# Optimization experiments

Hardware: AMD Instinct MI355X
Metric: run time of the kernel (lower is better)

## Reference

```python
import jax, jax.numpy as jnp
import numpy as np
import math


def butterfly_mult_untied(twiddle, x, increasing_stride=True):
    """twiddle: (nstack, m, n//2, 2, 2); x: (batch, nstack, n)."""
    b, nstack, n = x.shape
    m = twiddle.shape[1]
    out = x
    for idx in range(m):  # loop over log2(n) stages (structural, not data dim)
        log_stride = idx if increasing_stride else m - 1 - idx
        stride = 1 << log_stride
        nb = n // (2 * stride)
        # (nstack, nb, stride, 2, 2) -> (nstack, nb, 2, 2, stride)
        t = jnp.transpose(twiddle[:, idx].reshape(nstack, nb, stride, 2, 2), (0, 1, 3, 4, 2))
        o = out.reshape(b, nstack, nb, 1, 2, stride)
        out = (t * o).sum(axis=4).reshape(b, nstack, n)
    return out


def setup_inputs() -> dict:
    key = jax.random.key(0)
    k1, k2, k3 = jax.random.split(key, 3)
    batch, in_size, out_size = 32768, 1024, 1024
    m = int(math.ceil(math.log2(in_size)))  # 10
    nstack = 1
    x = jax.random.normal(k1, (batch, in_size), dtype=jnp.float32)
    # 'regular' non-ortho init: randn / sqrt(2)
    twiddle = jax.random.normal(k2, (nstack, m, in_size // 2, 2, 2), dtype=jnp.float32) / math.sqrt(2)
    bound = 1 / math.sqrt(in_size)
    bias = jax.random.uniform(k3, (out_size,), dtype=jnp.float32, minval=-bound, maxval=bound)
    return {"x": x, "twiddle": twiddle, "bias": bias}


def reference(x, twiddle, bias):
    batch, in_size = x.shape
    nstack = twiddle.shape[0]
    out_size = bias.shape[0]
    # pre_process: in_size is a power of 2 and nstack==1 -> just stack
    out = jnp.broadcast_to(x[:, None, :], (batch, nstack, in_size))
    out = butterfly_mult_untied(twiddle, out, increasing_stride=True)
    # post_process: flatten nstack, slice to out_size, add bias
    out = out.reshape(batch, nstack * in_size)[:, :out_size] + bias
    return out
```

## Files before the change

### kernel.cpp

```cpp
#include <hip/hip_runtime.h>


constexpr int N = 1024;
constexpr int B_ROWS = 4;
constexpr int WAVES = 4;

template<int STAGE>
__device__ __forceinline__ void do_stage(float2 (&v)[2][16],
                                         const float* __restrict__ tw,
                                         const int lane)
{
    constexpr int s = 1 << STAGE;
    const float* tws = tw + (STAGE << 11);

    if constexpr (s >= 4 && s <= 128) {
        constexpr int m = s >> 2;
        #pragma unroll
        for (int p = 0; p < 16; ++p) {
            const int e  = ((p >> 2) << 8) | (lane << 2) | (p & 3);
            const int i  = (e >> STAGE) & 1;
            const int pr = ((e >> (STAGE + 1)) << STAGE) | (e & (s - 1));
            const float2 tt = *(const float2*)(tws + pr * 4 + i * 2);
            const float tA = i ? tt.y : tt.x;
            const float tB = i ? tt.x : tt.y;
            #pragma unroll
            for (int q = 0; q < 2; ++q) {
                const float px = __shfl_xor(v[q][p].x, m, 64);
                const float py = __shfl_xor(v[q][p].y, m, 64);
                v[q][p].x = tA * v[q][p].x + tB * px;
                v[q][p].y = tA * v[q][p].y + tB * py;
            }
        }
    } else {
        constexpr int pm = (s == 1) ? 1 : (s == 2) ? 2 : (s == 256) ? 4 : 8;
        #pragma unroll
        for (int p = 0; p < 16; ++p) {
            if (p & pm) continue;
            const int p2 = p | pm;
            const int e  = ((p >> 2) << 8) | (lane << 2) | (p & 3);
            const int pr = ((e >> (STAGE + 1)) << STAGE) | (e & (s - 1));
            const float4 t4 = *(const float4*)(tws + pr * 4);
            #pragma unroll
            for (int q = 0; q < 2; ++q) {
                const float2 a = v[q][p];
                const float2 b = v[q][p2];
                v[q][p].x  = t4.x * a.x + t4.y * b.x;
                v[q][p].y  = t4.x * a.y + t4.y * b.y;
                v[q][p2].x = t4.z * a.x + t4.w * b.x;
                v[q][p2].y = t4.z * a.y + t4.w * b.y;
            }
        }
    }
}

__global__ __launch_bounds__(256, 2)
void butterfly_kernel(const float* __restrict__ x,
                      const float* __restrict__ tw,
                      const float* __restrict__ bias,
                      float* __restrict__ out)
{
    const int lane  = threadIdx.x & 63;
    const int waveg = blockIdx.x * WAVES + (threadIdx.x >> 6);
    const size_t row0 = (size_t)waveg * B_ROWS;

    float2 v[2][16];

    #pragma unroll
    for (int q = 0; q < 2; ++q) {
        const float* p0 = x + (row0 + 2 * q) * N + lane * 4;
        const float* p1 = p0 + N;
        #pragma unroll
        for (int r = 0; r < 4; ++r) {
            const float4 a = *(const float4*)(p0 + r * 256);
            const float4 b = *(const float4*)(p1 + r * 256);
            v[q][r * 4 + 0] = make_float2(a.x, b.x);
            v[q][r * 4 + 1] = make_float2(a.y, b.y);
            v[q][r * 4 + 2] = make_float2(a.z, b.z);
            v[q][r * 4 + 3] = make_float2(a.w, b.w);
        }
    }

    do_stage<0>(v, tw, lane);
    do_stage<1>(v, tw, lane);
    do_stage<2>(v, tw, lane);
    do_stage<3>(v, tw, lane);
    do_stage<4>(v, tw, lane);
    do_stage<5>(v, tw, lane);
    do_stage<6>(v, tw, lane);
    do_stage<7>(v, tw, lane);
    do_stage<8>(v, tw, lane);
    do_stage<9>(v, tw, lane);

    #pragma unroll
    for (int q = 0; q < 2; ++q) {
        float* o0 = out + (row0 + 2 * q) * N + lane * 4;
        float* o1 = o0 + N;
        #pragma unroll
        for (int r = 0; r < 4; ++r) {
            const float4 bb = *(const float4*)(bias + r * 256 + lane * 4);
            float4 a, b;
            a.x = v[q][r * 4 + 0].x + bb.x;  b.x = v[q][r * 4 + 0].y + bb.x;
            a.y = v[q][r * 4 + 1].x + bb.y;  b.y = v[q][r * 4 + 1].y + bb.y;
            a.z = v[q][r * 4 + 2].x + bb.z;  b.z = v[q][r * 4 + 2].y + bb.z;
            a.w = v[q][r * 4 + 3].x + bb.w;  b.w = v[q][r * 4 + 3].y + bb.w;
            *(float4*)(o0 + r * 256) = a;
            *(float4*)(o1 + r * 256) = b;
        }
    }
}

extern "C" void kernel_launch(void* const* d_in, const int* in_sizes, int n_in,
                              void* d_out, int out_size, void* d_ws, size_t ws_size,
                              hipStream_t stream) {
    const float* x    = (const float*)d_in[0];
    const float* tw   = (const float*)d_in[1];
    const float* bias = (const float*)d_in[2];
    float* out        = (float*)d_out;

    const int batch = in_sizes[0] / N;
    const int blocks = batch / (B_ROWS * WAVES);
    hipLaunchKernelGGL(butterfly_kernel, dim3(blocks), dim3(256), 0, stream,
                       x, tw, bias, out);
}
```

Measured before the change: 282.7 us.

## Stage twiddles in shared memory and double-buffer row chunks per wave

Each block now precomputes the pre-swapped twiddle pairs for stages 2-7 into a 48KB LDS table, so those stages do one contiguous float2 LDS read instead of index arithmetic plus a global load and select. Each wave processes four chunks of four rows with two register buffers, loading the next chunk while computing the current one, and the bias is loaded once per wave. Blocks grow from 16 to 64 rows and launch bounds drop to one block per SIMD. This doubles register pressure and LDS use, which may lower occupancy, and adds the table-building cost to every block.

```diff
diff --git a/kernel.cpp b/kernel.cpp
--- a/kernel.cpp
+++ b/kernel.cpp
@@ -2,37 +2,36 @@
 
 
 constexpr int N = 1024;
-constexpr int B_ROWS = 4;
-constexpr int WAVES = 4;
+constexpr int CHUNKS = 4;
+constexpr int ROWS_PER_CHUNK = 16;
+constexpr int ROWS_PER_BLOCK = CHUNKS * ROWS_PER_CHUNK;
+
 
 template<int STAGE>
 __device__ __forceinline__ void do_stage(float2 (&v)[2][16],
+                                         const float* __restrict__ tl,
                                          const float* __restrict__ tw,
                                          const int lane)
 {
     constexpr int s = 1 << STAGE;
-    const float* tws = tw + (STAGE << 11);
 
     if constexpr (s >= 4 && s <= 128) {
         constexpr int m = s >> 2;
+        const float* base = tl + (STAGE - 2) * 2048;
         #pragma unroll
         for (int p = 0; p < 16; ++p) {
-            const int e  = ((p >> 2) << 8) | (lane << 2) | (p & 3);
-            const int i  = (e >> STAGE) & 1;
-            const int pr = ((e >> (STAGE + 1)) << STAGE) | (e & (s - 1));
-            const float2 tt = *(const float2*)(tws + pr * 4 + i * 2);
-            const float tA = i ? tt.y : tt.x;
-            const float tB = i ? tt.x : tt.y;
+            const float2 tt = *(const float2*)(base + (((p << 6) | lane) << 1));
             #pragma unroll
             for (int q = 0; q < 2; ++q) {
                 const float px = __shfl_xor(v[q][p].x, m, 64);
                 const float py = __shfl_xor(v[q][p].y, m, 64);
-                v[q][p].x = tA * v[q][p].x + tB * px;
-                v[q][p].y = tA * v[q][p].y + tB * py;
+                v[q][p].x = tt.x * v[q][p].x + tt.y * px;
+                v[q][p].y = tt.x * v[q][p].y + tt.y * py;
             }
         }
     } else {
         constexpr int pm = (s == 1) ? 1 : (s == 2) ? 2 : (s == 256) ? 4 : 8;
+        const float* tws = tw + (STAGE << 11);
         #pragma unroll
         for (int p = 0; p < 16; ++p) {
             if (p & pm) continue;
@@ -53,18 +52,10 @@
     }
 }
 
-__global__ __launch_bounds__(256, 2)
-void butterfly_kernel(const float* __restrict__ x,
-                      const float* __restrict__ tw,
-                      const float* __restrict__ bias,
-                      float* __restrict__ out)
+__device__ __forceinline__ void load_rows(float2 (&v)[2][16],
+                                          const float* __restrict__ x,
+                                          const size_t row0, const int lane)
 {
-    const int lane  = threadIdx.x & 63;
-    const int waveg = blockIdx.x * WAVES + (threadIdx.x >> 6);
-    const size_t row0 = (size_t)waveg * B_ROWS;
-
-    float2 v[2][16];
-
     #pragma unroll
     for (int q = 0; q < 2; ++q) {
         const float* p0 = x + (row0 + 2 * q) * N + lane * 4;
@@ -79,17 +70,25 @@
             v[q][r * 4 + 3] = make_float2(a.w, b.w);
         }
     }
+}
 
-    do_stage<0>(v, tw, lane);
-    do_stage<1>(v, tw, lane);
-    do_stage<2>(v, tw, lane);
-    do_stage<3>(v, tw, lane);
-    do_stage<4>(v, tw, lane);
-    do_stage<5>(v, tw, lane);
-    do_stage<6>(v, tw, lane);
-    do_stage<7>(v, tw, lane);
-    do_stage<8>(v, tw, lane);
-    do_stage<9>(v, tw, lane);
+__device__ __forceinline__ void compute_store(float2 (&v)[2][16],
+                                              const float* __restrict__ tl,
+                                              const float* __restrict__ tw,
+                                              float* __restrict__ out,
+                                              const size_t row0, const int lane,
+                                              const float4 (&bb)[4])
+{
+    do_stage<0>(v, tl, tw, lane);
+    do_stage<1>(v, tl, tw, lane);
+    do_stage<2>(v, tl, tw, lane);
+    do_stage<3>(v, tl, tw, lane);
+    do_stage<4>(v, tl, tw, lane);
+    do_stage<5>(v, tl, tw, lane);
+    do_stage<6>(v, tl, tw, lane);
+    do_stage<7>(v, tl, tw, lane);
+    do_stage<8>(v, tl, tw, lane);
+    do_stage<9>(v, tl, tw, lane);
 
     #pragma unroll
     for (int q = 0; q < 2; ++q) {
@@ -97,16 +96,62 @@
         float* o1 = o0 + N;
         #pragma unroll
         for (int r = 0; r < 4; ++r) {
-            const float4 bb = *(const float4*)(bias + r * 256 + lane * 4);
             float4 a, b;
-            a.x = v[q][r * 4 + 0].x + bb.x;  b.x = v[q][r * 4 + 0].y + bb.x;
-            a.y = v[q][r * 4 + 1].x + bb.y;  b.y = v[q][r * 4 + 1].y + bb.y;
-            a.z = v[q][r * 4 + 2].x + bb.z;  b.z = v[q][r * 4 + 2].y + bb.z;
-            a.w = v[q][r * 4 + 3].x + bb.w;  b.w = v[q][r * 4 + 3].y + bb.w;
+            a.x = v[q][r * 4 + 0].x + bb[r].x;  b.x = v[q][r * 4 + 0].y + bb[r].x;
+            a.y = v[q][r * 4 + 1].x + bb[r].y;  b.y = v[q][r * 4 + 1].y + bb[r].y;
+            a.z = v[q][r * 4 + 2].x + bb[r].z;  b.z = v[q][r * 4 + 2].y + bb[r].z;
+            a.w = v[q][r * 4 + 3].x + bb[r].w;  b.w = v[q][r * 4 + 3].y + bb[r].w;
             *(float4*)(o0 + r * 256) = a;
             *(float4*)(o1 + r * 256) = b;
         }
     }
+}
+
+__global__ __launch_bounds__(256, 1)
+void butterfly_kernel(const float* __restrict__ x,
+                      const float* __restrict__ tw,
+                      const float* __restrict__ bias,
+                      float* __restrict__ out)
+{
+    __shared__ __align__(16) float tl[6 * 2048];
+
+    const int t    = threadIdx.x;
+    const int lane = t & 63;
+    const int g    = t >> 6;
+
+    #pragma unroll
+    for (int st = 2; st <= 7; ++st) {
+        const int s = 1 << st;
+        #pragma unroll
+        for (int k = 0; k < 4; ++k) {
+            const int p  = (g << 2) | k;
+            const int e  = ((p >> 2) << 8) | (lane << 2) | (p & 3);
+            const int i  = (e >> st) & 1;
+            const int pr = ((e >> (st + 1)) << st) | (e & (s - 1));
+            const float2 tt = *(const float2*)(tw + (st << 11) + pr * 4 + i * 2);
+            const float2 w  = i ? make_float2(tt.y, tt.x) : tt;
+            *(float2*)(tl + (st - 2) * 2048 + (((p << 6) | lane) << 1)) = w;
+        }
+    }
+
+    float4 bb[4];
+    #pragma unroll
+    for (int r = 0; r < 4; ++r)
+        bb[r] = *(const float4*)(bias + r * 256 + lane * 4);
+
+    __syncthreads();
+
+    const size_t base = (size_t)blockIdx.x * ROWS_PER_BLOCK + (size_t)(g * 4);
+
+    float2 vA[2][16], vB[2][16];
+    load_rows(vA, x, base + 0 * ROWS_PER_CHUNK, lane);
+    load_rows(vB, x, base + 1 * ROWS_PER_CHUNK, lane);
+    compute_store(vA, tl, tw, out, base + 0 * ROWS_PER_CHUNK, lane, bb);
+    load_rows(vA, x, base + 2 * ROWS_PER_CHUNK, lane);
+    compute_store(vB, tl, tw, out, base + 1 * ROWS_PER_CHUNK, lane, bb);
+    load_rows(vB, x, base + 3 * ROWS_PER_CHUNK, lane);
+    compute_store(vA, tl, tw, out, base + 2 * ROWS_PER_CHUNK, lane, bb);
+    compute_store(vB, tl, tw, out, base + 3 * ROWS_PER_CHUNK, lane, bb);
 }
 
 extern "C" void kernel_launch(void* const* d_in, const int* in_sizes, int n_in,
@@ -117,8 +162,8 @@
     const float* bias = (const float*)d_in[2];
     float* out        = (float*)d_out;
 
-    const int batch = in_sizes[0] / N;
-    const int blocks = batch / (B_ROWS * WAVES);
+    const int batch  = in_sizes[0] / N;
+    const int blocks = batch / ROWS_PER_BLOCK;
     hipLaunchKernelGGL(butterfly_kernel, dim3(blocks), dim3(256), 0, stream,
                        x, tw, bias, out);
 }
```

Measured after the change: 593.6 us. 110% more time.

## Replace wave shuffles with per-wave LDS transposes between butterfly stage groups

Applied to the files above, without the earlier changes.

Each lane now holds 16 contiguous elements per row, so stages 0-3 run entirely in registers. Two padded LDS transposes inside each wave's private buffer regroup the data so that stages 4-7 and then 8-9 are also register-local. This removes the many cross-lane shuffle instructions and the per-element twiddle selects of the old layout. In exchange it adds LDS traffic and about 21KB of shared memory per block, and it relies on wave-synchronous LDS access with no barrier.

```diff
diff --git a/kernel.cpp b/kernel.cpp
--- a/kernel.cpp
+++ b/kernel.cpp
@@ -4,51 +4,78 @@
 constexpr int N = 1024;
 constexpr int B_ROWS = 4;
 constexpr int WAVES = 4;
+constexpr int WBUF  = 1344;
 
-template<int STAGE>
-__device__ __forceinline__ void do_stage(float2 (&v)[2][16],
-                                         const float* __restrict__ tw,
-                                         const int lane)
+
+template<int ST>
+__device__ __forceinline__ void stageA(float (&v)[4][16],
+                                       const float4* __restrict__ tw4,
+                                       const int lane)
 {
-    constexpr int s = 1 << STAGE;
-    const float* tws = tw + (STAGE << 11);
+    constexpr int s = 1 << ST;
+    #pragma unroll
+    for (int pi = 0; pi < 8; ++pi) {
+        const int jl = ((pi >> ST) << (ST + 1)) | (pi & (s - 1));
+        const int jh = jl + s;
+        const int e  = 16 * lane + jl;
+        const int pr = ((e >> (ST + 1)) << ST) | (e & (s - 1));
+        const float4 t = tw4[ST * 512 + pr];
+        #pragma unroll
+        for (int r = 0; r < 4; ++r) {
+            const float lo = v[r][jl], hi = v[r][jh];
+            v[r][jl] = t.x * lo + t.y * hi;
+            v[r][jh] = t.z * lo + t.w * hi;
+        }
+    }
+}
 
-    if constexpr (s >= 4 && s <= 128) {
-        constexpr int m = s >> 2;
+template<int ST>
+__device__ __forceinline__ void stageE(float (&v)[4][16],
+                                       const float4* __restrict__ tw4,
+                                       const int lane)
+{
+    constexpr int s  = 1 << ST;
+    constexpr int km = 1 << (ST - 4);
+    const int a = lane >> 4, b = lane & 15;
+    #pragma unroll
+    for (int pi = 0; pi < 8; ++pi) {
+        const int kl = ((pi >> (ST - 4)) << (ST - 3)) | (pi & (km - 1));
+        const int kh = kl + km;
+        const int e  = 256 * a + 16 * kl + b;
+        const int pr = ((e >> (ST + 1)) << ST) | (e & (s - 1));
+        const float4 t = tw4[ST * 512 + pr];
         #pragma unroll
-        for (int p = 0; p < 16; ++p) {
-            const int e  = ((p >> 2) << 8) | (lane << 2) | (p & 3);
-            const int i  = (e >> STAGE) & 1;
-            const int pr = ((e >> (STAGE + 1)) << STAGE) | (e & (s - 1));
-            const float2 tt = *(const float2*)(tws + pr * 4 + i * 2);
-            const float tA = i ? tt.y : tt.x;
-            const float tB = i ? tt.x : tt.y;
-            #pragma unroll
-            for (int q = 0; q < 2; ++q) {
-                const float px = __shfl_xor(v[q][p].x, m, 64);
-                const float py = __shfl_xor(v[q][p].y, m, 64);
-                v[q][p].x = tA * v[q][p].x + tB * px;
-                v[q][p].y = tA * v[q][p].y + tB * py;
-            }
+        for (int r = 0; r < 4; ++r) {
+            const float lo = v[r][kl], hi = v[r][kh];
+            v[r][kl] = t.x * lo + t.y * hi;
+            v[r][kh] = t.z * lo + t.w * hi;
         }
-    } else {
-        constexpr int pm = (s == 1) ? 1 : (s == 2) ? 2 : (s == 256) ? 4 : 8;
+    }
+}
+
+template<int ST>
+__device__ __forceinline__ void stageF(float (&v)[4][16],
+                                       const float4* __restrict__ tw4,
+                                       const int lane)
+{
+    constexpr int s  = 1 << ST;
+    constexpr int am = 1 << (ST - 8);
+    #pragma unroll
+    for (int pi = 0; pi < 8; ++pi) {
+        const int ai   = pi >> 2;
+        const int b10  = pi & 3;
+        const int a_lo = ((ai >> (ST - 8)) << (ST - 7)) | (ai & (am - 1));
+        const int a_hi = a_lo + am;
+        const int ml   = a_lo * 4 + b10;
+        const int mh   = a_hi * 4 + b10;
+        const int e    = a_lo * 256 + 4 * lane + b10;
+        const int pr   = ((e >> (ST + 1)) << ST) | (e & (s - 1));
+        const float4 t = tw4[ST * 512 + pr];
         #pragma unroll
-        for (int p = 0; p < 16; ++p) {
-            if (p & pm) continue;
-            const int p2 = p | pm;
-            const int e  = ((p >> 2) << 8) | (lane << 2) | (p & 3);
-            const int pr = ((e >> (STAGE + 1)) << STAGE) | (e & (s - 1));
-            const float4 t4 = *(const float4*)(tws + pr * 4);
-            #pragma unroll
-            for (int q = 0; q < 2; ++q) {
-                const float2 a = v[q][p];
-                const float2 b = v[q][p2];
-                v[q][p].x  = t4.x * a.x + t4.y * b.x;
-                v[q][p].y  = t4.x * a.y + t4.y * b.y;
-                v[q][p2].x = t4.z * a.x + t4.w * b.x;
-                v[q][p2].y = t4.z * a.y + t4.w * b.y;
-            }
+        for (int r = 0; r < 4; ++r) {
+            const float lo = v[r][ml], hi = v[r][mh];
+            v[r][ml] = t.x * lo + t.y * hi;
+            v[r][mh] = t.z * lo + t.w * hi;
         }
     }
 }
@@ -59,52 +86,88 @@
                       const float* __restrict__ bias,
                       float* __restrict__ out)
 {
-    const int lane  = threadIdx.x & 63;
-    const int waveg = blockIdx.x * WAVES + (threadIdx.x >> 6);
-    const size_t row0 = (size_t)waveg * B_ROWS;
+    __shared__ __align__(16) float tl[WAVES][WBUF];
 
-    float2 v[2][16];
+    const int t    = threadIdx.x;
+    const int lane = t & 63;
+    const int g    = t >> 6;
+    float* wb = tl[g];
+
+    const size_t row0 = ((size_t)blockIdx.x * WAVES + g) * B_ROWS;
+    const float4* tw4 = (const float4*)tw;
+
+    float v[4][16];
 
     #pragma unroll
-    for (int q = 0; q < 2; ++q) {
-        const float* p0 = x + (row0 + 2 * q) * N + lane * 4;
-        const float* p1 = p0 + N;
+    for (int r = 0; r < 4; ++r) {
+        const float* px = x + (row0 + r) * N + 16 * lane;
         #pragma unroll
-        for (int r = 0; r < 4; ++r) {
-            const float4 a = *(const float4*)(p0 + r * 256);
-            const float4 b = *(const float4*)(p1 + r * 256);
-            v[q][r * 4 + 0] = make_float2(a.x, b.x);
-            v[q][r * 4 + 1] = make_float2(a.y, b.y);
-            v[q][r * 4 + 2] = make_float2(a.z, b.z);
-            v[q][r * 4 + 3] = make_float2(a.w, b.w);
+        for (int i = 0; i < 4; ++i) {
+            const float4 d = *(const float4*)(px + 4 * i);
+            v[r][4 * i + 0] = d.x; v[r][4 * i + 1] = d.y;
+            v[r][4 * i + 2] = d.z; v[r][4 * i + 3] = d.w;
         }
     }
 
-    do_stage<0>(v, tw, lane);
-    do_stage<1>(v, tw, lane);
-    do_stage<2>(v, tw, lane);
-    do_stage<3>(v, tw, lane);
-    do_stage<4>(v, tw, lane);
-    do_stage<5>(v, tw, lane);
-    do_stage<6>(v, tw, lane);
-    do_stage<7>(v, tw, lane);
-    do_stage<8>(v, tw, lane);
-    do_stage<9>(v, tw, lane);
+    stageA<0>(v, tw4, lane);
+    stageA<1>(v, tw4, lane);
+    stageA<2>(v, tw4, lane);
+    stageA<3>(v, tw4, lane);
+
+    {
+        const int wbase = 20 * lane + 16 * ((lane >> 4) & 3);
+        const int a = lane >> 4, b = lane & 15;
+        const int rb = 336 * a + b;
+        #pragma unroll
+        for (int r = 0; r < 4; ++r) {
+            #pragma unroll
+            for (int i = 0; i < 4; ++i)
+                *(float4*)(wb + wbase + 4 * i) =
+                    make_float4(v[r][4 * i + 0], v[r][4 * i + 1],
+                                v[r][4 * i + 2], v[r][4 * i + 3]);
+            #pragma unroll
+            for (int k = 0; k < 16; ++k)
+                v[r][k] = wb[rb + 20 * k];
+        }
+    }
+
+    stageE<4>(v, tw4, lane);
+    stageE<5>(v, tw4, lane);
+    stageE<6>(v, tw4, lane);
+    stageE<7>(v, tw4, lane);
+
+    {
+        const int a = lane >> 4, b = lane & 15;
+        const int wbase = 336 * a + 20 * b;
+        const int rb = 80 * (lane & 3) + (lane >> 2);
+        #pragma unroll
+        for (int r = 0; r < 4; ++r) {
+            #pragma unroll
+            for (int i = 0; i < 4; ++i)
+                *(float4*)(wb + wbase + 4 * i) =
+                    make_float4(v[r][4 * i + 0], v[r][4 * i + 1],
+                                v[r][4 * i + 2], v[r][4 * i + 3]);
+            #pragma unroll
+            for (int m = 0; m < 16; ++m)
+                v[r][m] = wb[rb + 336 * (m >> 2) + 20 * (m & 3)];
+        }
+    }
+
+    stageF<8>(v, tw4, lane);
+    stageF<9>(v, tw4, lane);
 
     #pragma unroll
-    for (int q = 0; q < 2; ++q) {
-        float* o0 = out + (row0 + 2 * q) * N + lane * 4;
-        float* o1 = o0 + N;
+    for (int r = 0; r < 4; ++r) {
+        float* po = out + (row0 + r) * N + 4 * lane;
         #pragma unroll
-        for (int r = 0; r < 4; ++r) {
-            const float4 bb = *(const float4*)(bias + r * 256 + lane * 4);
-            float4 a, b;
-            a.x = v[q][r * 4 + 0].x + bb.x;  b.x = v[q][r * 4 + 0].y + bb.x;
-            a.y = v[q][r * 4 + 1].x + bb.y;  b.y = v[q][r * 4 + 1].y + bb.y;
-            a.z = v[q][r * 4 + 2].x + bb.z;  b.z = v[q][r * 4 + 2].y + bb.z;
-            a.w = v[q][r * 4 + 3].x + bb.w;  b.w = v[q][r * 4 + 3].y + bb.w;
-            *(float4*)(o0 + r * 256) = a;
-            *(float4*)(o1 + r * 256) = b;
+        for (int aa = 0; aa < 4; ++aa) {
+            const float4 bb = *(const float4*)(bias + aa * 256 + 4 * lane);
+            float4 o;
+            o.x = v[r][4 * aa + 0] + bb.x;
+            o.y = v[r][4 * aa + 1] + bb.y;
+            o.z = v[r][4 * aa + 2] + bb.z;
+            o.w = v[r][4 * aa + 3] + bb.w;
+            *(float4*)(po + aa * 256) = o;
         }
     }
 }
@@ -117,7 +180,7 @@
     const float* bias = (const float*)d_in[2];
     float* out        = (float*)d_out;
 
-    const int batch = in_sizes[0] / N;
+    const int batch  = in_sizes[0] / N;
     const int blocks = batch / (B_ROWS * WAVES);
     hipLaunchKernelGGL(butterfly_kernel, dim3(blocks), dim3(256), 0, stream,
                        x, tw, bias, out);
```

After: 261.5 us. 1.08x faster.
